# Performance work log

Hardware: AMD Instinct MI355X
Metric: run time of the kernel (lower is better)

Reference implementation:

```python
import jax, jax.numpy as jnp
import numpy as np

B, S, D, H = 2, 2048, 512, 8
HD = D // H
EPS = 1e-8
SCALE = HD ** -0.5


def setup_inputs() -> dict:
    key = jax.random.key(0)
    ks = jax.random.split(key, 12)
    gene_emb = jax.random.normal(ks[0], (B, S, D), jnp.float32)
    expr_emb = jax.random.normal(ks[1], (B, S, D), jnp.float32)
    M = jax.random.randint(ks[2], (B, S, S), 0, 2).astype(jnp.float32)
    def lin(k, fan_in, fan_out):
        kw, kb = jax.random.split(k)
        bound = 1.0 / np.sqrt(fan_in)
        W = jax.random.uniform(kw, (fan_in, fan_out), jnp.float32, -bound, bound)
        b = jax.random.uniform(kb, (fan_out,), jnp.float32, -bound, bound)
        return W, b
    Wf, bf = lin(ks[3], 2 * D, D)  # fused_emb_proj
    Wq, bq = lin(ks[4], D, D)
    Wk, bk = lin(ks[5], D, D)
    Wv, bv = lin(ks[6], D, D)
    Wo, bo = lin(ks[7], D, D)
    return {"gene_emb": gene_emb, "expr_emb": expr_emb, "M": M,
            "Wf": Wf, "bf": bf, "Wq": Wq, "bq": bq, "Wk": Wk, "bk": bk,
            "Wv": Wv, "bv": bv, "Wo": Wo, "bo": bo}


def reference(gene_emb, expr_emb, M, Wf, bf, Wq, bq, Wk, bk, Wv, bv, Wo, bo):
    # fused=True, self_attention=False path: Q and K from projected concat
    fused = jnp.concatenate([gene_emb, expr_emb], axis=-1) @ Wf + bf  # [B,S,D]
    Q = (fused @ Wq + bq).reshape(B, S, H, HD)
    K = (fused @ Wk + bk).reshape(B, S, H, HD)
    V = (expr_emb @ Wv + bv).reshape(B, S, H, HD)
    scores = jnp.einsum('bqhd,bkhd->bhqk', Q, K) * SCALE  # [B,H,S,S]
    Mh = M[:, None, :, :]  # broadcast over heads
    scores = scores + jnp.where(Mh == 0, -1e9, 0.0)
    attn = jax.nn.softmax(scores, axis=-1)
    A = attn * Mh  # gated weights
    A = A / (jnp.sum(jnp.abs(A), axis=-1, keepdims=True) + EPS)  # abs-sum renorm
    out = jnp.einsum('bhqk,bkhd->bqhd', A, V).reshape(B, S, D)
    return out @ Wo + bo
```

## Files before the change

### kernel.cpp

```cpp
#include <hip/hip_runtime.h>
#include <stdint.h>
#include <math.h>

#define BB 2
#define SS 2048
#define DDIM 512
#define HH 8
#define HDD 64

typedef unsigned short u16;
typedef unsigned int u32;
typedef unsigned long long u64;
typedef short bf16x8 __attribute__((ext_vector_type(8)));
typedef float f32x4 __attribute__((ext_vector_type(4)));

__device__ __forceinline__ u16 f2bf(float x) {
  unsigned int u = __float_as_uint(x);
  unsigned int r = (u + 0x7fffu + ((u >> 16) & 1u)) >> 16;
  return (u16)r;
}

__device__ __forceinline__ u32 cvtpk(float a, float b) {
  u32 r;
  asm("v_cvt_pk_bf16_f32 %0, %1, %2" : "=v"(r) : "v"(a), "v"(b));
  return r;
}

__device__ __forceinline__ void cp16(const void* g, void* l) {
  __builtin_amdgcn_global_load_lds(
      (const __attribute__((address_space(1))) void*)g,
      (__attribute__((address_space(3))) void*)l, 16, 0, 0);
}

__global__ __launch_bounds__(256) void cast_bf16_k(
    const float* __restrict__ g, const float* __restrict__ e,
    u16* __restrict__ og, u16* __restrict__ oe) {
  int i = blockIdx.x * 256 + threadIdx.x;
  float4 a = ((const float4*)g)[i];
  float4 b = ((const float4*)e)[i];
  ushort4 ua, ub;
  ua.x = f2bf(a.x); ua.y = f2bf(a.y); ua.z = f2bf(a.z); ua.w = f2bf(a.w);
  ub.x = f2bf(b.x); ub.y = f2bf(b.y); ub.z = f2bf(b.z); ub.w = f2bf(b.w);
  ((ushort4*)og)[i] = ua;
  ((ushort4*)oe)[i] = ub;
}

__global__ __launch_bounds__(256) void wprep_k(
    const float* __restrict__ Wf, const float* __restrict__ Wq,
    const float* __restrict__ Wk, const float* __restrict__ Wv,
    const float* __restrict__ Wo,
    u16* __restrict__ WfT, u16* __restrict__ WqT, u16* __restrict__ WkT,
    u16* __restrict__ WvT, u16* __restrict__ WoT) {
  int z = blockIdx.z;
  const float* W; u16* WT; int K;
  switch (z) {
    case 0: W = Wf; WT = WfT; K = 1024; break;
    case 1: W = Wq; WT = WqT; K = 512; break;
    case 2: W = Wk; WT = WkT; K = 512; break;
    case 3: W = Wv; WT = WvT; K = 512; break;
    default: W = Wo; WT = WoT; K = 512; break;
  }
  int k0 = blockIdx.y * 32;
  if (k0 >= K) return;
  int n0 = blockIdx.x * 32;
  __shared__ float t[32][33];
  int tx = threadIdx.x & 31, ty = threadIdx.x >> 5;
#pragma unroll
  for (int i = 0; i < 32; i += 8)
    t[ty + i][tx] = W[(size_t)(k0 + ty + i) * DDIM + n0 + tx];
  __syncthreads();
#pragma unroll
  for (int i = 0; i < 32; i += 8)
    WT[(size_t)(n0 + ty + i) * K + k0 + tx] = f2bf(t[tx][ty + i]);
}

__global__ __launch_bounds__(256) void mpack2_k(const float* __restrict__ M,
                                                u64* __restrict__ Mp) {
  int wid = (blockIdx.x * 256 + threadIdx.x) >> 6;
  int lane = threadIdx.x & 63;
#pragma unroll 4
  for (int i = 0; i < 16; ++i) {
    int idx = wid * 16 + i;
    int row = idx >> 3, k = idx & 7;
    float4 v = *(const float4*)&M[(size_t)row * SS + k * 256 + lane * 4];
    u64 b0 = __ballot(v.x != 0.0f);
    u64 b1 = __ballot(v.y != 0.0f);
    u64 b2 = __ballot(v.z != 0.0f);
    u64 b3 = __ballot(v.w != 0.0f);
    if (lane == 0) {
      u64* p = Mp + ((size_t)row * 32 + k * 4);
      p[0] = b0; p[1] = b1; p[2] = b2; p[3] = b3;
    }
  }
}

template <int EPI>
__global__ __launch_bounds__(256) void gemm_k(
    const u16* __restrict__ A0, const u16* __restrict__ A1,
    const u16* __restrict__ Bt0, const u16* __restrict__ Bt1,
    const u16* __restrict__ Bt2,
    const float* __restrict__ bias0, const float* __restrict__ bias1,
    const float* __restrict__ bias2,
    u16* __restrict__ O0, u16* __restrict__ O1, u16* __restrict__ O2,
    float* __restrict__ OF) {
  constexpr int BK = 32;
  __shared__ alignas(16) u16 Al[64 * BK];
  __shared__ alignas(16) u16 Bl[64 * BK];

  const int tid = threadIdx.x;
  const int l = tid & 63, w = tid >> 6, lg = l >> 4, lr = l & 15;
  const int wm = w >> 1, wn = w & 1;
  const int m0 = blockIdx.y * 64;
  const int n0 = blockIdx.x * 64;
  const int Ksz = (EPI == 0) ? 1024 : 512;

  const u16* Aa = A0; const u16* Bt = Bt0; const float* bias = bias0;
  int z = 0;
  if (EPI == 1) {
    z = blockIdx.z;
    Aa = (z == 2) ? A1 : A0;
    Bt = (z == 0) ? Bt0 : (z == 1) ? Bt1 : Bt2;
    bias = (z == 0) ? bias0 : (z == 1) ? bias1 : bias2;
  }

  f32x4 zero4 = {0.f, 0.f, 0.f, 0.f};
  f32x4 acc[2][2];
#pragma unroll
  for (int i = 0; i < 2; ++i)
#pragma unroll
    for (int j = 0; j < 2; ++j) acc[i][j] = zero4;

  const int arow = tid >> 2;
  const int apos = tid & 3;
  const int k8s = apos ^ ((arow >> 1) & 3);

  for (int k0 = 0; k0 < Ksz; k0 += BK) {
    __syncthreads();
    {
      int kg = k0 + 8 * k8s;
      const u16* src;
      if (EPI == 0) {
        src = (kg < 512) ? (A0 + (size_t)(m0 + arow) * 512 + kg)
                         : (A1 + (size_t)(m0 + arow) * 512 + (kg - 512));
      } else {
        src = Aa + (size_t)(m0 + arow) * 512 + kg;
      }
      cp16(src, (char*)Al + (size_t)arow * 64 + apos * 16);
    }
    {
      const u16* src = Bt + (size_t)(n0 + arow) * Ksz + k0 + 8 * k8s;
      cp16(src, (char*)Bl + (size_t)arow * 64 + apos * 16);
    }
    asm volatile("s_waitcnt vmcnt(0)" ::: "memory");
    __syncthreads();

    bf16x8 af[2], bfr[2];
#pragma unroll
    for (int i = 0; i < 2; ++i) {
      int row = 32 * wm + 16 * i + lr;
      af[i] = *(const bf16x8*)((const char*)Al + row * 64 +
                               ((lg ^ ((row >> 1) & 3)) * 16));
    }
#pragma unroll
    for (int j = 0; j < 2; ++j) {
      int row = 32 * wn + 16 * j + lr;
      bfr[j] = *(const bf16x8*)((const char*)Bl + row * 64 +
                                ((lg ^ ((row >> 1) & 3)) * 16));
    }
#pragma unroll
    for (int i = 0; i < 2; ++i)
#pragma unroll
      for (int j = 0; j < 2; ++j)
        acc[i][j] =
            __builtin_amdgcn_mfma_f32_16x16x32_bf16(af[i], bfr[j], acc[i][j], 0, 0, 0);
  }

#pragma unroll
  for (int j = 0; j < 2; ++j) {
    int c = n0 + 32 * wn + 16 * j + lr;
    float bv = bias[c];
#pragma unroll
    for (int i = 0; i < 2; ++i) {
      int qb = m0 + 32 * wm + 16 * i + 4 * lg;
      if (EPI == 0) {
#pragma unroll
        for (int r = 0; r < 4; ++r)
          O0[(size_t)(qb + r) * 512 + c] = f2bf(acc[i][j][r] + bv);
      } else if (EPI == 2) {
#pragma unroll
        for (int r = 0; r < 4; ++r)
          OF[(size_t)(qb + r) * 512 + c] = acc[i][j][r] + bv;
      } else {
        int b = qb >> 11, s = qb & 2047;
        int hh = c >> 6, hd = c & 63;
        if (z < 2) {
          const float qsc = (z == 0) ? 0.18033688011112042f : 1.0f;
          u16* O = (z == 0) ? O0 : O1;
#pragma unroll
          for (int r = 0; r < 4; ++r)
            O[((size_t)(b * HH + hh) * SS + s + r) * HDD + hd] =
                f2bf((acc[i][j][r] + bv) * qsc);
        } else {
          ushort4 v;
          v.x = f2bf(acc[i][j][0] + bv);
          v.y = f2bf(acc[i][j][1] + bv);
          v.z = f2bf(acc[i][j][2] + bv);
          v.w = f2bf(acc[i][j][3] + bv);
          *(ushort4*)(O2 + ((size_t)(b * HH + hh) * HDD + hd) * SS + s) = v;
        }
      }
    }
  }
}

__global__ __launch_bounds__(256) void attn5_k(
    const u16* __restrict__ Qh, const u16* __restrict__ Kh,
    const u16* __restrict__ Vt, const u64* __restrict__ Mp,
    u16* __restrict__ AO) {
  __shared__ alignas(16) u16 Kl[2][64 * 64];
  __shared__ alignas(16) u16 Vl[2][64 * 64];
  __shared__ alignas(16) u16 Pl[4][16 * 64];

  const int tid = threadIdx.x;
  const int l = tid & 63, w = tid >> 6, lg = l >> 4, lr = l & 15;
  const int bh = blockIdx.y, b = bh >> 3, h = bh & 7;
  const int qw = blockIdx.x * 64 + 16 * w;

  bf16x8 qf0, qf1;
  {
    const u16* qp = Qh + ((size_t)bh * SS + qw + lr) * HDD + 8 * lg;
    qf0 = *(const bf16x8*)qp;
    qf1 = *(const bf16x8*)(qp + 32);
  }

  f32x4 zero4 = {0.f, 0.f, 0.f, 0.f};
  f32x4 o[4];
#pragma unroll
  for (int t4 = 0; t4 < 4; ++t4) o[t4] = zero4;
  float mrun = -INFINITY, lrun = 0.f;

  const u64* Mrow = Mp + ((size_t)b * SS + qw + lr) * 32;
  u64 mp[4], mpN[4];
#pragma unroll
  for (int r = 0; r < 4; ++r) mp[r] = Mrow[r];

  int kOff[4][2], vOff[4][2], pOff[2], wOff[4];
#pragma unroll
  for (int g = 0; g < 4; ++g) {
    int krow = 16 * g + lr;
    kOff[g][0] = krow * 128 + ((lg ^ (krow & 7)) * 16);
    kOff[g][1] = krow * 128 + (((4 + lg) ^ (krow & 7)) * 16);
  }
#pragma unroll
  for (int t4 = 0; t4 < 4; ++t4) {
    int vrow = 16 * t4 + lr;
    vOff[t4][0] = vrow * 128 + ((lg ^ (vrow & 7)) * 16);
    vOff[t4][1] = vrow * 128 + (((4 + lg) ^ (vrow & 7)) * 16);
  }
#pragma unroll
  for (int kk = 0; kk < 2; ++kk)
    pOff[kk] = lr * 128 + (((4 * kk + lg) ^ (lr & 7)) * 16);
#pragma unroll
  for (int g = 0; g < 4; ++g)
    wOff[g] = lr * 128 + (((2 * g + (lg >> 1)) ^ (lr & 7)) * 16) + (lg & 1) * 8;

  const int srow = tid >> 3, spos = tid & 7;
  const int sk8 = spos ^ (srow & 7);
  const size_t sdst = (size_t)tid * 16;
  const u16* pK0 = Kh + ((size_t)bh * SS + srow) * HDD + 8 * sk8;
  const u16* pK1 = pK0 + 32 * HDD;
  const u16* pV0 = Vt + ((size_t)bh * HDD + srow) * SS + 8 * sk8;
  const u16* pV1 = pV0 + 32 * SS;

  cp16(pK0, (char*)Kl[0] + sdst);
  cp16(pK1, (char*)Kl[0] + sdst + 4096);
  cp16(pV0, (char*)Vl[0] + sdst);
  cp16(pV1, (char*)Vl[0] + sdst + 4096);
  asm volatile("s_waitcnt vmcnt(0)" ::: "memory");
  __syncthreads();

  u16* Pw = Pl[w];
  int cur = 0;
  for (int kt = 0; kt < 32; ++kt) {
    if (kt < 31) {
      pK0 += 64 * HDD; pK1 += 64 * HDD; pV0 += 64; pV1 += 64;
      char* kd = (char*)Kl[cur ^ 1];
      char* vd = (char*)Vl[cur ^ 1];
      cp16(pK0, kd + sdst);
      cp16(pK1, kd + sdst + 4096);
      cp16(pV0, vd + sdst);
      cp16(pV1, vd + sdst + 4096);
    }
    const int tm = kt & 3;
    if (tm == 0 && kt < 28) {
#pragma unroll
      for (int r = 0; r < 4; ++r) mpN[r] = Mrow[((kt >> 2) + 1) * 4 + r];
    }

    const char* Klw = (const char*)Kl[cur];
    const char* Vlw = (const char*)Vl[cur];

    f32x4 sc[4];
#pragma unroll
    for (int g = 0; g < 4; ++g) {
      bf16x8 k0f = *(const bf16x8*)(Klw + kOff[g][0]);
      bf16x8 k1f = *(const bf16x8*)(Klw + kOff[g][1]);
      f32x4 zz = zero4;
      zz = __builtin_amdgcn_mfma_f32_16x16x32_bf16(k0f, qf0, zz, 0, 0, 0);
      zz = __builtin_amdgcn_mfma_f32_16x16x32_bf16(k1f, qf1, zz, 0, 0, 0);
      sc[g] = zz;
    }
    {
      u32 wb[4];
#pragma unroll
      for (int r = 0; r < 4; ++r) wb[r] = (u32)(mp[r] >> (16 * tm + lg));
#pragma unroll
      for (int g = 0; g < 4; ++g)
#pragma unroll
        for (int r = 0; r < 4; ++r)
          if (!((wb[r] >> (4 * g)) & 1u)) sc[g][r] = -INFINITY;
    }
    float t = sc[0][0];
#pragma unroll
    for (int g = 0; g < 4; ++g)
#pragma unroll
      for (int r = 0; r < 4; ++r) t = fmaxf(t, sc[g][r]);
    t = fmaxf(t, __shfl_xor(t, 16));
    t = fmaxf(t, __shfl_xor(t, 32));
    float mnew = fmaxf(mrun, t);
    float fac = (mnew == -INFINITY) ? 1.0f : exp2f(mrun - mnew);
    float msafe = fmaxf(mnew, -1e30f);
    float psum = 0.f;
#pragma unroll
    for (int g = 0; g < 4; ++g)
#pragma unroll
      for (int r = 0; r < 4; ++r) {
        float p = exp2f(sc[g][r] - msafe);
        sc[g][r] = p;
        psum += p;
      }
    psum += __shfl_xor(psum, 16);
    psum += __shfl_xor(psum, 32);
    mrun = mnew;
    lrun = lrun * fac + psum;
#pragma unroll
    for (int t4 = 0; t4 < 4; ++t4) o[t4] *= fac;
#pragma unroll
    for (int g = 0; g < 4; ++g) {
      uint2 pv;
      pv.x = cvtpk(sc[g][0], sc[g][1]);
      pv.y = cvtpk(sc[g][2], sc[g][3]);
      *(uint2*)((char*)Pw + wOff[g]) = pv;
    }
#pragma unroll
    for (int kk = 0; kk < 2; ++kk) {
      bf16x8 pf = *(const bf16x8*)((const char*)Pw + pOff[kk]);
#pragma unroll
      for (int t4 = 0; t4 < 4; ++t4) {
        bf16x8 vf = *(const bf16x8*)(Vlw + vOff[t4][kk]);
        o[t4] = __builtin_amdgcn_mfma_f32_16x16x32_bf16(vf, pf, o[t4], 0, 0, 0);
      }
    }
    if (tm == 3) {
#pragma unroll
      for (int r = 0; r < 4; ++r) mp[r] = mpN[r];
    }
    asm volatile("s_waitcnt vmcnt(0)" ::: "memory");
    __syncthreads();
    cur ^= 1;
  }

  float inv = (lrun > 0.f) ? 1.0f / (lrun + 1e-8f) : 0.f;
  u16* op = AO + ((size_t)b * SS + qw + lr) * DDIM + h * HDD + 4 * lg;
#pragma unroll
  for (int t4 = 0; t4 < 4; ++t4) {
    ushort4 v;
    v.x = f2bf(o[t4][0] * inv);
    v.y = f2bf(o[t4][1] * inv);
    v.z = f2bf(o[t4][2] * inv);
    v.w = f2bf(o[t4][3] * inv);
    *(ushort4*)(op + 16 * t4) = v;
  }
}

extern "C" void kernel_launch(void* const* d_in, const int* in_sizes, int n_in,
                              void* d_out, int out_size, void* d_ws, size_t ws_size,
                              hipStream_t stream) {
  if (ws_size < (size_t)(31.5 * 1024 * 1024)) return;

  const float* gene = (const float*)d_in[0];
  const float* expr = (const float*)d_in[1];
  const float* Mm = (const float*)d_in[2];
  const float* Wf = (const float*)d_in[3];
  const float* bf = (const float*)d_in[4];
  const float* Wq = (const float*)d_in[5];
  const float* bq = (const float*)d_in[6];
  const float* Wk = (const float*)d_in[7];
  const float* bk = (const float*)d_in[8];
  const float* Wv = (const float*)d_in[9];
  const float* bv = (const float*)d_in[10];
  const float* Wo = (const float*)d_in[11];
  const float* bo = (const float*)d_in[12];
  float* out = (float*)d_out;

  char* ws = (char*)d_ws;
  const size_t MB4 = 4194304;
  u16* geneB = (u16*)(ws + 0 * MB4);
  u16* exprB = (u16*)(ws + 1 * MB4);
  u16* fusedB = (u16*)(ws + 2 * MB4);
  u16* QhB = (u16*)(ws + 3 * MB4);
  u16* KhB = (u16*)(ws + 4 * MB4);
  u16* VtB = (u16*)(ws + 5 * MB4);
  u16* attnB = (u16*)(ws + 6 * MB4);
  u16* WfT = (u16*)(ws + 7 * MB4);
  u16* WqT = (u16*)(ws + 7 * MB4 + 1048576);
  u16* WkT = (u16*)(ws + 7 * MB4 + 1048576 + 524288);
  u16* WvT = (u16*)(ws + 7 * MB4 + 1048576 + 2 * 524288);
  u16* WoT = (u16*)(ws + 7 * MB4 + 1048576 + 3 * 524288);
  u64* MpB = (u64*)(ws + 0 * MB4);

  cast_bf16_k<<<2048, 256, 0, stream>>>(gene, expr, geneB, exprB);
  wprep_k<<<dim3(16, 32, 5), 256, 0, stream>>>(Wf, Wq, Wk, Wv, Wo, WfT, WqT,
                                               WkT, WvT, WoT);
  gemm_k<0><<<dim3(8, 64), 256, 0, stream>>>(geneB, exprB, WfT, nullptr, nullptr,
                                             bf, nullptr, nullptr, fusedB,
                                             nullptr, nullptr, nullptr);
  mpack2_k<<<512, 256, 0, stream>>>(Mm, MpB);
  gemm_k<1><<<dim3(8, 64, 3), 256, 0, stream>>>(fusedB, exprB, WqT, WkT, WvT,
                                                bq, bk, bv, QhB, KhB, VtB,
                                                nullptr);
  attn5_k<<<dim3(32, 16), 256, 0, stream>>>(QhB, KhB, VtB, MpB, attnB);
  gemm_k<2><<<dim3(8, 64), 256, 0, stream>>>(attnB, nullptr, WoT, nullptr,
                                             nullptr, bo, nullptr, nullptr,
                                             nullptr, nullptr, nullptr, out);
}
```

Before: 219.0 us.

## Double-buffer GEMM shared tiles and widen K step to 64

Replaces the single-buffered BK=32 GEMM loop with a double-buffered BK=64 loop. The next tile's async global-to-LDS copies are issued before the MFMAs on the current tile run, and the XOR swizzle is redone for 128-byte rows. This halves the number of barrier round-trips and overlaps load latency with compute, at the cost of four times the LDS per block, which may reduce occupancy.

```diff
diff --git a/kernel.cpp b/kernel.cpp
--- a/kernel.cpp
+++ b/kernel.cpp
@@ -95,7 +95,7 @@
 }
 
 template <int EPI>
-__global__ __launch_bounds__(256) void gemm_k(
+__global__ __launch_bounds__(256) void gemm2_k(
     const u16* __restrict__ A0, const u16* __restrict__ A1,
     const u16* __restrict__ Bt0, const u16* __restrict__ Bt1,
     const u16* __restrict__ Bt2,
@@ -103,16 +103,16 @@
     const float* __restrict__ bias2,
     u16* __restrict__ O0, u16* __restrict__ O1, u16* __restrict__ O2,
     float* __restrict__ OF) {
-  constexpr int BK = 32;
-  __shared__ alignas(16) u16 Al[64 * BK];
-  __shared__ alignas(16) u16 Bl[64 * BK];
+  constexpr int KSZ = (EPI == 0) ? 1024 : 512;
+  constexpr int NIT = KSZ / 64;
+  __shared__ alignas(16) u16 Al[2][64 * 64];
+  __shared__ alignas(16) u16 Bl[2][64 * 64];
 
   const int tid = threadIdx.x;
   const int l = tid & 63, w = tid >> 6, lg = l >> 4, lr = l & 15;
   const int wm = w >> 1, wn = w & 1;
   const int m0 = blockIdx.y * 64;
   const int n0 = blockIdx.x * 64;
-  const int Ksz = (EPI == 0) ? 1024 : 512;
 
   const u16* Aa = A0; const u16* Bt = Bt0; const float* bias = bias0;
   int z = 0;
@@ -130,49 +130,72 @@
 #pragma unroll
     for (int j = 0; j < 2; ++j) acc[i][j] = zero4;
 
-  const int arow = tid >> 2;
-  const int apos = tid & 3;
-  const int k8s = apos ^ ((arow >> 1) & 3);
-
-  for (int k0 = 0; k0 < Ksz; k0 += BK) {
-    __syncthreads();
-    {
-      int kg = k0 + 8 * k8s;
-      const u16* src;
-      if (EPI == 0) {
-        src = (kg < 512) ? (A0 + (size_t)(m0 + arow) * 512 + kg)
-                         : (A1 + (size_t)(m0 + arow) * 512 + (kg - 512));
-      } else {
-        src = Aa + (size_t)(m0 + arow) * 512 + kg;
-      }
-      cp16(src, (char*)Al + (size_t)arow * 64 + apos * 16);
-    }
-    {
-      const u16* src = Bt + (size_t)(n0 + arow) * Ksz + k0 + 8 * k8s;
-      cp16(src, (char*)Bl + (size_t)arow * 64 + apos * 16);
-    }
+  const int srow = tid >> 3, spos = tid & 7;
+  const int sk8 = spos ^ (srow & 7);
+  const size_t sdst = (size_t)tid * 16;
+
+  int aOff[2][2], bOff[2][2];
+#pragma unroll
+  for (int i = 0; i < 2; ++i) {
+    int row = 32 * wm + 16 * i + lr;
+    aOff[i][0] = row * 128 + ((lg ^ (row & 7)) * 16);
+    aOff[i][1] = row * 128 + (((4 + lg) ^ (row & 7)) * 16);
+  }
+#pragma unroll
+  for (int j = 0; j < 2; ++j) {
+    int row = 32 * wn + 16 * j + lr;
+    bOff[j][0] = row * 128 + ((lg ^ (row & 7)) * 16);
+    bOff[j][1] = row * 128 + (((4 + lg) ^ (row & 7)) * 16);
+  }
+
+  auto STAGE = [&](int buf, int kt) {
+    int kbase = kt * 64 + 8 * sk8;
+    const u16* sA;
+    if (EPI == 0) {
+      const u16* Asrc = (kt < 8) ? A0 : A1;
+      int kk = (kt < 8) ? kbase : kbase - 512;
+      sA = Asrc + (size_t)(m0 + srow) * 512 + kk;
+    } else {
+      sA = Aa + (size_t)(m0 + srow) * 512 + kbase;
+    }
+    const u16* sB = Bt + (size_t)(n0 + srow) * KSZ + kbase;
+    cp16(sA, (char*)Al[buf] + sdst);
+    cp16(sA + 32 * 512, (char*)Al[buf] + sdst + 4096);
+    cp16(sB, (char*)Bl[buf] + sdst);
+    cp16(sB + 32 * KSZ, (char*)Bl[buf] + sdst + 4096);
+  };
+
+  STAGE(0, 0);
+  asm volatile("s_waitcnt vmcnt(0)" ::: "memory");
+  __syncthreads();
+
+  int cur = 0;
+  for (int kt = 0; kt < NIT; ++kt) {
+    if (kt + 1 < NIT) STAGE(cur ^ 1, kt + 1);
+    const char* Ab = (const char*)Al[cur];
+    const char* Bb = (const char*)Bl[cur];
+    bf16x8 af[2][2], bfr[2][2];
+#pragma unroll
+    for (int i = 0; i < 2; ++i) {
+      af[i][0] = *(const bf16x8*)(Ab + aOff[i][0]);
+      af[i][1] = *(const bf16x8*)(Ab + aOff[i][1]);
+    }
+#pragma unroll
+    for (int j = 0; j < 2; ++j) {
+      bfr[j][0] = *(const bf16x8*)(Bb + bOff[j][0]);
+      bfr[j][1] = *(const bf16x8*)(Bb + bOff[j][1]);
+    }
+#pragma unroll
+    for (int kk = 0; kk < 2; ++kk)
+#pragma unroll
+      for (int i = 0; i < 2; ++i)
+#pragma unroll
+        for (int j = 0; j < 2; ++j)
+          acc[i][j] = __builtin_amdgcn_mfma_f32_16x16x32_bf16(
+              af[i][kk], bfr[j][kk], acc[i][j], 0, 0, 0);
     asm volatile("s_waitcnt vmcnt(0)" ::: "memory");
     __syncthreads();
-
-    bf16x8 af[2], bfr[2];
-#pragma unroll
-    for (int i = 0; i < 2; ++i) {
-      int row = 32 * wm + 16 * i + lr;
-      af[i] = *(const bf16x8*)((const char*)Al + row * 64 +
-                               ((lg ^ ((row >> 1) & 3)) * 16));
-    }
-#pragma unroll
-    for (int j = 0; j < 2; ++j) {
-      int row = 32 * wn + 16 * j + lr;
-      bfr[j] = *(const bf16x8*)((const char*)Bl + row * 64 +
-                                ((lg ^ ((row >> 1) & 3)) * 16));
-    }
-#pragma unroll
-    for (int i = 0; i < 2; ++i)
-#pragma unroll
-      for (int j = 0; j < 2; ++j)
-        acc[i][j] =
-            __builtin_amdgcn_mfma_f32_16x16x32_bf16(af[i], bfr[j], acc[i][j], 0, 0, 0);
+    cur ^= 1;
   }
 
 #pragma unroll
@@ -422,15 +445,15 @@
   cast_bf16_k<<<2048, 256, 0, stream>>>(gene, expr, geneB, exprB);
   wprep_k<<<dim3(16, 32, 5), 256, 0, stream>>>(Wf, Wq, Wk, Wv, Wo, WfT, WqT,
                                                WkT, WvT, WoT);
-  gemm_k<0><<<dim3(8, 64), 256, 0, stream>>>(geneB, exprB, WfT, nullptr, nullptr,
-                                             bf, nullptr, nullptr, fusedB,
-                                             nullptr, nullptr, nullptr);
+  gemm2_k<0><<<dim3(8, 64), 256, 0, stream>>>(geneB, exprB, WfT, nullptr, nullptr,
+                                              bf, nullptr, nullptr, fusedB,
+                                              nullptr, nullptr, nullptr);
   mpack2_k<<<512, 256, 0, stream>>>(Mm, MpB);
-  gemm_k<1><<<dim3(8, 64, 3), 256, 0, stream>>>(fusedB, exprB, WqT, WkT, WvT,
-                                                bq, bk, bv, QhB, KhB, VtB,
-                                                nullptr);
+  gemm2_k<1><<<dim3(8, 64, 3), 256, 0, stream>>>(fusedB, exprB, WqT, WkT, WvT,
+                                                 bq, bk, bv, QhB, KhB, VtB,
+                                                 nullptr);
   attn5_k<<<dim3(32, 16), 256, 0, stream>>>(QhB, KhB, VtB, MpB, attnB);
-  gemm_k<2><<<dim3(8, 64), 256, 0, stream>>>(attnB, nullptr, WoT, nullptr,
-                                             nullptr, bo, nullptr, nullptr,
-                                             nullptr, nullptr, nullptr, out);
-}
+  gemm2_k<2><<<dim3(8, 64), 256, 0, stream>>>(attnB, nullptr, WoT, nullptr,
+                                              nullptr, bo, nullptr, nullptr,
+                                              nullptr, nullptr, nullptr, out);
+}
```

After: 225.6 us. +3.0%, slower.
